# Performance work log

Hardware: AMD Instinct MI355X
Metric: run time of the kernel (lower is better)

Reference implementation:

```python
import jax, jax.numpy as jnp
import numpy as np

B, T, C, NH = 32, 512, 1024, 16
DH = C // NH


def _rope_tables(seq_len, dim):
    # matches RotaryEmbedding: inv_freq over even indices; emb=cat(freqs,freqs),
    # but only the first dim//2 columns (== freqs) are ever sliced out.
    inv = 1.0 / (10000.0 ** (np.arange(0, dim, 2, dtype=np.float32) / dim))
    freqs = np.arange(seq_len, dtype=np.float32)[:, None] * inv[None, :]  # [T, dh/2]
    return jnp.asarray(np.cos(freqs)), jnp.asarray(np.sin(freqs))


def _apply_rope(x, cos, sin):
    # x: [B,T,H,D] with D even; interleaved-pair rotation as in the torch code
    b, t, h, d = x.shape
    d2 = d // 2
    xv = x.reshape(b, t, h, d2, 2)
    x0, x1 = xv[..., 0], xv[..., 1]
    c = cos[None, :t, None, :]  # [1,T,1,d2]
    s = sin[None, :t, None, :]
    o0 = x0 * c - x1 * s
    o1 = x0 * s + x1 * c
    return jnp.stack([o0, o1], axis=-1).reshape(b, t, h, d)


def setup_inputs() -> dict:
    key = jax.random.key(0)
    ks = jax.random.split(key, 5)
    scale = 0.02
    return {
        "x": jax.random.normal(ks[0], (B, T, C), dtype=jnp.float32),
        "Wq": jax.random.normal(ks[1], (C, C), dtype=jnp.float32) * scale,
        "Wk": jax.random.normal(ks[2], (C, C), dtype=jnp.float32) * scale,
        "Wv": jax.random.normal(ks[3], (C, C), dtype=jnp.float32) * scale,
        "Wo": jax.random.normal(ks[4], (C, C), dtype=jnp.float32) * scale,
    }


def reference(x, Wq, Wk, Wv, Wo):
    b, t, c = x.shape
    cos, sin = _rope_tables(t, DH)
    # torch nn.Linear(bias=False): y = x @ W.T
    q = (x @ Wq.T).reshape(b, t, NH, DH)
    k = (x @ Wk.T).reshape(b, t, NH, DH)
    v = (x @ Wv.T).reshape(b, t, NH, DH)
    q = _apply_rope(q, cos, sin)
    k = _apply_rope(k, cos, sin)
    # [B,H,T,D]
    q = q.transpose(0, 2, 1, 3)
    k = k.transpose(0, 2, 1, 3)
    v = v.transpose(0, 2, 1, 3)
    # fp32 scores + fp32 softmax (explicit, matches the torch upcast)
    att = jnp.einsum("bhqd,bhkd->bhqk", q.astype(jnp.float32), k.astype(jnp.float32))
    att = att * (DH ** -0.5)
    att = jax.nn.softmax(att, axis=-1).astype(v.dtype)
    # dropout omitted (eval mode)
    out = jnp.einsum("bhqk,bhkd->bhqd", att, v)
    out = out.transpose(0, 2, 1, 3).reshape(b, t, c)
    return out @ Wo.T
```

## Files before the change

### kernel.cpp

```cpp
#include <hip/hip_runtime.h>
#include <hip/hip_bf16.h>
#include <stdint.h>

#define B_  32
#define T_  512
#define C_  1024
#define NH_ 16
#define DH_ 64

typedef __attribute__((ext_vector_type(8))) __bf16 bf16x8;
typedef __attribute__((ext_vector_type(4))) __bf16 bf16x4;
typedef __attribute__((ext_vector_type(4))) float  f32x4;

__device__ __forceinline__ void gload_lds16(const void* g, void* lds) {
  __builtin_amdgcn_global_load_lds(
      (const __attribute__((address_space(1))) void*)(uintptr_t)g,
      (__attribute__((address_space(3))) void*)(uint32_t)(uintptr_t)lds,
      16, 0, 0);
}

__global__ void prep_kernel(const float* __restrict__ x,
                            const float* __restrict__ Wq, const float* __restrict__ Wk,
                            const float* __restrict__ Wv, const float* __restrict__ Wo,
                            __bf16* __restrict__ xb, __bf16* __restrict__ wqkv,
                            __bf16* __restrict__ wob,
                            float* __restrict__ cosT, float* __restrict__ sinT) {
  int i = blockIdx.x * blockDim.x + threadIdx.x;
  if (i < 4194304) {
    f32x4 v = *(const f32x4*)(x + (size_t)i * 4);
    bf16x4 o;
    o[0] = (__bf16)v[0]; o[1] = (__bf16)v[1]; o[2] = (__bf16)v[2]; o[3] = (__bf16)v[3];
    *(bf16x4*)(xb + (size_t)i * 4) = o;
  } else if (i < 5242880) {
    int j = i - 4194304;
    int w = j >> 18, idx = j & 262143;
    const float* src = (w == 0) ? Wq : (w == 1) ? Wk : (w == 2) ? Wv : Wo;
    __bf16* dst = (w == 3) ? wob : wqkv + (size_t)w * 1048576;
    f32x4 v = *(const f32x4*)(src + (size_t)idx * 4);
    bf16x4 o;
    o[0] = (__bf16)v[0]; o[1] = (__bf16)v[1]; o[2] = (__bf16)v[2]; o[3] = (__bf16)v[3];
    *(bf16x4*)(dst + (size_t)idx * 4) = o;
  } else if (i < 5259264) {
    int j = i - 5242880;
    int t = j >> 5, f = j & 31;
    float inv = powf(10000.0f, -(float)(2 * f) / 64.0f);
    float fr = (float)t * inv;
    cosT[j] = cosf(fr);
    sinT[j] = sinf(fr);
  }
}

template <int MODE>
__global__ __launch_bounds__(512, 2) void gemm8(
    const __bf16* __restrict__ A,
    const __bf16* __restrict__ W0, const __bf16* __restrict__ W1, const __bf16* __restrict__ W2,
    __bf16* __restrict__ q, __bf16* __restrict__ k, __bf16* __restrict__ vt,
    float* __restrict__ outp) {
  extern __shared__ __bf16 lds[];
  const int K = C_;
  const int NH8 = 64;
  int tid = threadIdx.x;
  int lane = tid & 63, wave = tid >> 6;
  int ql = lane & 15, g = lane >> 4;
  int wr = wave >> 2, wc = wave & 3;

  constexpr int BNH = (MODE == 0) ? 6 : 2;
  int bid = blockIdx.x;
  int xcd = bid & 7, local = bid >> 3;
  int bm = (xcd >> 1) * 16 + local / BNH;
  int bn = (xcd & 1) * BNH + local % BNH;

  const __bf16* Ag = A + (size_t)bm * 256 * K;
  const __bf16* Wg;
  if (MODE == 0) {
    int mat = bn >> 2;
    const __bf16* Wsel = (mat == 0) ? W0 : (mat == 1) ? W1 : W2;
    Wg = Wsel + (size_t)(bn & 3) * 256 * K;
  } else {
    Wg = W0 + (size_t)bn * 256 * K;
  }

  int schunk = (tid & 3) ^ ((tid >> 3) & 3);
  size_t stg_base = (size_t)(tid >> 2) * K + schunk * 8;

  int xsw = (g ^ ((ql >> 1) & 3)) * 8;
  int aoffW[8], boffW[4];
#pragma unroll
  for (int m = 0; m < 8; m++) aoffW[m] = (wr * 128 + m * 16 + ql) * 32 + xsw;
#pragma unroll
  for (int n = 0; n < 4; n++) boffW[n] = (wc * 64 + n * 16 + ql) * 32 + xsw;

#define STAGE_H(h)                                                          \
  if ((h) < NH8) {                                                          \
    int tl_ = (h) >> 2, pt_ = (h) & 3;                                      \
    const __bf16* s_ = ((pt_ & 1) ? Wg : Ag) + stg_base +                   \
                       (size_t)tl_ * 64 + (pt_ >> 1) * 32;                  \
    __bf16* d_ = lds + (((tl_ & 1) * 4 + pt_) * 8192) + tid * 8;            \
    gload_lds16(s_, d_);                                                    \
    gload_lds16(s_ + (size_t)128 * K, d_ + 4096);                           \
  }

#define PH(TP, KK, MLO, RB, SH, VM)                                         \
  {                                                                         \
    const __bf16* abase_ = lds + (((TP) * 4 + ((KK) ? 2 : 0)) * 8192);      \
    _Pragma("unroll")                                                       \
    for (int mm = 0; mm < 4; mm++)                                          \
      a[mm] = *(const bf16x8*)(abase_ + aoffW[(MLO) + mm]);                 \
    if (RB) {                                                               \
      const __bf16* bbase_ = lds + (((TP) * 4 + ((KK) ? 3 : 1)) * 8192);    \
      _Pragma("unroll")                                                     \
      for (int n = 0; n < 4; n++)                                           \
        b[n] = *(const bf16x8*)(bbase_ + boffW[n]);                         \
    }                                                                       \
    STAGE_H(SH);                                                            \
    __builtin_amdgcn_s_barrier();                                           \
    asm volatile("s_waitcnt lgkmcnt(0)" ::: "memory");                      \
    __builtin_amdgcn_sched_barrier(0);                                      \
    __builtin_amdgcn_s_setprio(1);                                          \
    _Pragma("unroll")                                                       \
    for (int mm = 0; mm < 4; mm++)                                          \
      _Pragma("unroll")                                                     \
      for (int n = 0; n < 4; n++)                                           \
        acc[(MLO) + mm][n] = __builtin_amdgcn_mfma_f32_16x16x32_bf16(       \
            a[mm], b[n], acc[(MLO) + mm][n], 0, 0, 0);                      \
    __builtin_amdgcn_s_setprio(0);                                          \
    {                                                                       \
      int vm_ = (VM);                                                       \
      if (vm_ == 0)      { asm volatile("s_waitcnt vmcnt(0)" ::: "memory"); } \
      else if (vm_ > 0)  { asm volatile("s_waitcnt vmcnt(6)" ::: "memory"); } \
    }                                                                       \
    __builtin_amdgcn_s_barrier();                                           \
  }

  STAGE_H(0); STAGE_H(1); STAGE_H(2); STAGE_H(3);
  STAGE_H(4); STAGE_H(5); STAGE_H(6);
  asm volatile("s_waitcnt vmcnt(6)" ::: "memory");
  __builtin_amdgcn_s_barrier();
  __builtin_amdgcn_sched_barrier(0);

  f32x4 acc[8][4] = {};
  bf16x8 a[4], b[4];
  for (int i = 0; i < 8; ++i) {
    int hb = 8 * i;
    int vm4 = (i == 7) ? 0 : 6;
    int vm8 = (i == 7) ? -1 : 6;
    PH(0, 0, 0, 1, hb + 7,  -1)
    PH(0, 0, 4, 0, hb + 8,  -1)
    PH(0, 1, 0, 1, hb + 9,  -1)
    PH(0, 1, 4, 0, hb + 10, vm4)
    PH(1, 0, 0, 1, hb + 11, -1)
    PH(1, 0, 4, 0, hb + 12, -1)
    PH(1, 1, 0, 1, hb + 13, -1)
    PH(1, 1, 4, 0, hb + 14, vm8)
  }
#undef PH
#undef STAGE_H

  int r0 = bm * 256 + wr * 128;
  int c0 = bn * 256 + wc * 64;
  if (MODE == 0) {
    int mat = c0 >> 10;
#pragma unroll
    for (int m = 0; m < 8; m++) {
      int row = r0 + m * 16 + g * 4;
      int bb = row >> 9, tt = row & 511;
#pragma unroll
      for (int n = 0; n < 4; n++) {
        int col = c0 + n * 16 + ql;
        int h = (col & 1023) >> 6, d = col & 63;
        if (mat == 2) {
          bf16x4 ov;
#pragma unroll
          for (int r = 0; r < 4; r++) ov[r] = (__bf16)acc[m][n][r];
          *(bf16x4*)(vt + ((size_t)(bb * NH_ + h) * DH_ + d) * T_ + tt) = ov;
        } else {
          __bf16* dst = (mat == 0 ? q : k) + ((size_t)(bb * NH_ + h) * T_ + tt) * DH_ + d;
#pragma unroll
          for (int r = 0; r < 4; r++) dst[r * DH_] = (__bf16)acc[m][n][r];
        }
      }
    }
  } else {
#pragma unroll
    for (int m = 0; m < 8; m++) {
      int row = r0 + m * 16 + g * 4;
#pragma unroll
      for (int r = 0; r < 4; r++)
#pragma unroll
        for (int n = 0; n < 4; n++)
          outp[(size_t)(row + r) * C_ + c0 + n * 16 + ql] = acc[m][n][r];
    }
  }
}

__global__ __launch_bounds__(512, 2) void attn_kernel(
    const __bf16* __restrict__ qg, const __bf16* __restrict__ kg,
    const __bf16* __restrict__ vg, __bf16* __restrict__ ao,
    const float* __restrict__ cosT, const float* __restrict__ sinT) {
  extern __shared__ char smem[];
  __bf16* Klds = (__bf16*)smem;
  __bf16* Vlds = (__bf16*)(smem + 65536);

  int tid = threadIdx.x;
  int lane = tid & 63, wave = tid >> 6;
  int ql = lane & 15, g = lane >> 4;
  int bh = blockIdx.x;
  int b = bh >> 4, h = bh & 15;
  const __bf16* qp = qg + (size_t)bh * (T_ * DH_);
  const __bf16* kp = kg + (size_t)bh * (T_ * DH_);
  const __bf16* vp = vg + (size_t)bh * (T_ * DH_);

  {
    int cb = tid & 7;
    int rb = tid >> 3;
#pragma unroll
    for (int i = 0; i < 8; i++) {
      int row = rb + i * 64;
      bf16x8 raw = *(const bf16x8*)(kp + (size_t)row * DH_ + cb * 8);
      f32x4 c4 = *(const f32x4*)(cosT + row * 32 + cb * 4);
      f32x4 s4 = *(const f32x4*)(sinT + row * 32 + cb * 4);
      bf16x8 out;
#pragma unroll
      for (int p = 0; p < 4; p++) {
        float a0 = (float)raw[2 * p], a1 = (float)raw[2 * p + 1];
        out[2 * p]     = (__bf16)(a0 * c4[p] - a1 * s4[p]);
        out[2 * p + 1] = (__bf16)(a0 * s4[p] + a1 * c4[p]);
      }
      *(bf16x8*)(Klds + row * 64 + ((cb ^ (row & 7)) * 8)) = out;
    }
  }
  {
    int d = tid >> 3;
    int cb = tid & 7;
    const __bf16* vrow = vp + (size_t)d * T_;
#pragma unroll
    for (int i = 0; i < 8; i++) {
      int c8 = cb + i * 8;
      bf16x8 raw = *(const bf16x8*)(vrow + c8 * 8);
      *(bf16x8*)(Vlds + d * 516 + c8 * 8) = raw;
    }
  }

  int q0 = wave * 64;
  bf16x8 qf[4][2];
#pragma unroll
  for (int s = 0; s < 4; s++)
#pragma unroll
    for (int kk = 0; kk < 2; kk++) {
      int tq = q0 + s * 16 + ql;
      bf16x8 raw = *(const bf16x8*)(qp + (size_t)tq * DH_ + kk * 32 + g * 8);
      int fb = tq * 32 + kk * 16 + g * 4;
      f32x4 c4 = *(const f32x4*)(cosT + fb);
      f32x4 s4 = *(const f32x4*)(sinT + fb);
      bf16x8 out;
#pragma unroll
      for (int p = 0; p < 4; p++) {
        float a0 = (float)raw[2 * p], a1 = (float)raw[2 * p + 1];
        out[2 * p]     = (__bf16)(0.125f * (a0 * c4[p] - a1 * s4[p]));
        out[2 * p + 1] = (__bf16)(0.125f * (a0 * s4[p] + a1 * c4[p]));
      }
      qf[s][kk] = out;
    }

  __syncthreads();

  f32x4 o[4][4] = {};
  float mrow[4] = {-1e30f, -1e30f, -1e30f, -1e30f};
  float lrow[4] = {0.f, 0.f, 0.f, 0.f};

  for (int kv0 = 0; kv0 < T_; kv0 += 32) {
    bf16x8 kf[2][2], vf[4];
#pragma unroll
    for (int sub = 0; sub < 2; sub++)
#pragma unroll
      for (int kk = 0; kk < 2; kk++) {
        int t = kv0 + sub * 16 + ql;
        int cc = kk * 4 + g;
        kf[sub][kk] = *(const bf16x8*)(Klds + t * 64 + ((cc ^ (t & 7)) * 8));
      }
#pragma unroll
    for (int c = 0; c < 4; c++) {
      int d = c * 16 + ql;
      bf16x4 vlo = *(const bf16x4*)(Vlds + d * 516 + kv0 + g * 4);
      bf16x4 vhi = *(const bf16x4*)(Vlds + d * 516 + kv0 + 16 + g * 4);
#pragma unroll
      for (int r = 0; r < 4; r++) { vf[c][r] = vlo[r]; vf[c][4 + r] = vhi[r]; }
    }

#pragma unroll
    for (int s = 0; s < 4; s++) {
      f32x4 s0 = {0.f, 0.f, 0.f, 0.f}, s1 = {0.f, 0.f, 0.f, 0.f};
      __builtin_amdgcn_s_setprio(1);
#pragma unroll
      for (int kk = 0; kk < 2; kk++) {
        s0 = __builtin_amdgcn_mfma_f32_16x16x32_bf16(kf[0][kk], qf[s][kk], s0, 0, 0, 0);
        s1 = __builtin_amdgcn_mfma_f32_16x16x32_bf16(kf[1][kk], qf[s][kk], s1, 0, 0, 0);
      }
      __builtin_amdgcn_s_setprio(0);
      float tm = s0[0];
#pragma unroll
      for (int r = 1; r < 4; r++) tm = fmaxf(tm, s0[r]);
#pragma unroll
      for (int r = 0; r < 4; r++) tm = fmaxf(tm, s1[r]);
      tm = fmaxf(tm, __shfl_xor(tm, 16));
      tm = fmaxf(tm, __shfl_xor(tm, 32));
      if (!__all(tm <= mrow[s] + 8.0f)) {
        float mnew = fmaxf(mrow[s], tm);
        float corr = __expf(mrow[s] - mnew);
        mrow[s] = mnew;
        lrow[s] *= corr;
#pragma unroll
        for (int c = 0; c < 4; c++) o[s][c] *= corr;
      }
      float p0[4], p1[4], ps = 0.f;
#pragma unroll
      for (int r = 0; r < 4; r++) {
        p0[r] = __expf(s0[r] - mrow[s]);
        p1[r] = __expf(s1[r] - mrow[s]);
        ps += p0[r] + p1[r];
      }
      ps += __shfl_xor(ps, 16);
      ps += __shfl_xor(ps, 32);
      lrow[s] += ps;
      bf16x8 pb;
#pragma unroll
      for (int r = 0; r < 4; r++) {
        pb[r]     = (__bf16)p0[r];
        pb[4 + r] = (__bf16)p1[r];
      }
      __builtin_amdgcn_s_setprio(1);
#pragma unroll
      for (int c = 0; c < 4; c++)
        o[s][c] = __builtin_amdgcn_mfma_f32_16x16x32_bf16(vf[c], pb, o[s][c], 0, 0, 0);
      __builtin_amdgcn_s_setprio(0);
    }
  }

#pragma unroll
  for (int s = 0; s < 4; s++) {
    float inv = 1.0f / lrow[s];
    size_t row = (size_t)b * T_ + q0 + s * 16 + ql;
    size_t baseo = row * C_ + h * DH_;
#pragma unroll
    for (int c = 0; c < 4; c++) {
      bf16x4 ov;
#pragma unroll
      for (int r = 0; r < 4; r++) ov[r] = (__bf16)(o[s][c][r] * inv);
      *(bf16x4*)(ao + baseo + c * 16 + g * 4) = ov;
    }
  }
}

extern "C" void kernel_launch(void* const* d_in, const int* in_sizes, int n_in,
                              void* d_out, int out_size, void* d_ws, size_t ws_size,
                              hipStream_t stream) {
  (void)in_sizes; (void)n_in; (void)out_size; (void)ws_size;
  const float* x  = (const float*)d_in[0];
  const float* Wq = (const float*)d_in[1];
  const float* Wk = (const float*)d_in[2];
  const float* Wv = (const float*)d_in[3];
  const float* Wo = (const float*)d_in[4];

  char* ws = (char*)d_ws;
  char* od = (char*)d_out;
  float* outp = (float*)d_out;

  __bf16* qb = (__bf16*)(od);
  __bf16* kb = (__bf16*)(od + 33554432);
  __bf16* xb   = (__bf16*)(ws);
  __bf16* vtb  = (__bf16*)(ws + 33554432);
  __bf16* wqkv = (__bf16*)(ws + 67108864);
  __bf16* wob  = (__bf16*)(ws + 73400320);
  float*  cosT = (float*)(ws + 75497472);
  float*  sinT = (float*)(ws + 75563008);
  __bf16* aob  = xb;

  auto k0 = gemm8<0>; auto k1 = gemm8<1>;
  hipFuncSetAttribute((const void*)k0, hipFuncAttributeMaxDynamicSharedMemorySize, 131072);
  hipFuncSetAttribute((const void*)k1, hipFuncAttributeMaxDynamicSharedMemorySize, 131072);
  hipFuncSetAttribute((const void*)attn_kernel, hipFuncAttributeMaxDynamicSharedMemorySize, 131584);

  prep_kernel<<<dim3(20544), dim3(256), 0, stream>>>(
      x, Wq, Wk, Wv, Wo, xb, wqkv, wob, cosT, sinT);

  gemm8<0><<<dim3(768), dim3(512), 131072, stream>>>(
      xb, wqkv, wqkv + 1048576, wqkv + 2097152, qb, kb, vtb, nullptr);

  attn_kernel<<<dim3(B_ * NH_), dim3(512), 131584, stream>>>(
      qb, kb, vtb, aob, cosT, sinT);

  gemm8<1><<<dim3(256), dim3(512), 131072, stream>>>(
      aob, wob, nullptr, nullptr, nullptr, nullptr, nullptr, outp);
}
```

Baseline: 254.8 us.

## Add smaller-tile output projection GEMM and async swizzled V loads in attention

The output projection moves to a new 128x128-tile GEMM kernel with 256 threads, 1024 blocks and XCD-aware block mapping. The aim is better CU occupancy and load balance than the 256-block gemm8<1> launch gave. In attention, V is now staged into LDS with direct global-to-LDS loads using an XOR swizzle instead of a padded row stride, which cuts register round trips and trims LDS to 128 KiB. The new GEMM has no double buffering, so its loads and MFMAs may serialize.

Measured after the change: 265.4 us. 1.04x slower.

```diff
diff --git a/kernel.cpp b/kernel.cpp
--- a/kernel.cpp
+++ b/kernel.cpp
@@ -193,6 +193,68 @@
   }
 }
 
+__global__ __launch_bounds__(256) void gemm_op(
+    const __bf16* __restrict__ A, const __bf16* __restrict__ W,
+    float* __restrict__ outp) {
+  __shared__ __bf16 As[128 * 64];
+  __shared__ __bf16 Bs[128 * 64];
+  const int K = C_;
+  int tid = threadIdx.x;
+  int lane = tid & 63, wave = tid >> 6;
+  int ql = lane & 15, g = lane >> 4;
+  int wr = wave >> 1, wc = wave & 1;
+
+  int xcd = blockIdx.x & 7, local = blockIdx.x >> 3;
+  int bm = xcd * 16 + (local >> 3);
+  int bn = local & 7;
+
+  int srow = tid >> 3;
+  int cphys = tid & 7;
+  int clog = cphys ^ (srow & 7);
+  const __bf16* Ab = A + (size_t)(bm * 128 + srow) * K + clog * 8;
+  const __bf16* Wb = W + (size_t)(bn * 128 + srow) * K + clog * 8;
+  __bf16* AsP = &As[srow * 64 + cphys * 8];
+  __bf16* BsP = &Bs[srow * 64 + cphys * 8];
+
+  int xk = ql & 7;
+  f32x4 acc[4][4] = {};
+  for (int k0 = 0; k0 < K; k0 += 64) {
+#pragma unroll
+    for (int i = 0; i < 4; i++) gload_lds16(Ab + (size_t)i * 32 * K + k0, AsP + i * 2048);
+#pragma unroll
+    for (int i = 0; i < 4; i++) gload_lds16(Wb + (size_t)i * 32 * K + k0, BsP + i * 2048);
+    __syncthreads();
+#pragma unroll
+    for (int kk = 0; kk < 2; kk++) {
+      bf16x8 a[4], b[4];
+#pragma unroll
+      for (int m = 0; m < 4; m++)
+        a[m] = *(const bf16x8*)&As[(wr * 64 + m * 16 + ql) * 64 + (((kk * 4 + g) ^ xk) * 8)];
+#pragma unroll
+      for (int n = 0; n < 4; n++)
+        b[n] = *(const bf16x8*)&Bs[(wc * 64 + n * 16 + ql) * 64 + (((kk * 4 + g) ^ xk) * 8)];
+#pragma unroll
+      for (int m = 0; m < 4; m++)
+#pragma unroll
+        for (int n = 0; n < 4; n++)
+          acc[m][n] = __builtin_amdgcn_mfma_f32_16x16x32_bf16(a[m], b[n], acc[m][n], 0, 0, 0);
+    }
+    __syncthreads();
+  }
+
+  int r0 = bm * 128 + wr * 64;
+  int c0 = bn * 128 + wc * 64;
+#pragma unroll
+  for (int m = 0; m < 4; m++) {
+    int row = r0 + m * 16 + g * 4;
+#pragma unroll
+    for (int r = 0; r < 4; r++)
+#pragma unroll
+      for (int n = 0; n < 4; n++)
+        outp[(size_t)(row + r) * C_ + c0 + n * 16 + ql] = acc[m][n][r];
+  }
+}
+
 __global__ __launch_bounds__(512, 2) void attn_kernel(
     const __bf16* __restrict__ qg, const __bf16* __restrict__ kg,
     const __bf16* __restrict__ vg, __bf16* __restrict__ ao,
@@ -210,6 +272,13 @@
   const __bf16* kp = kg + (size_t)bh * (T_ * DH_);
   const __bf16* vp = vg + (size_t)bh * (T_ * DH_);
 
+#pragma unroll
+  for (int i = 0; i < 8; i++) {
+    int d = i * 8 + wave;
+    const __bf16* src = vp + (size_t)d * T_ + ((lane ^ wave) * 8);
+    gload_lds16(src, Vlds + d * 512 + lane * 8);
+  }
+
   {
     int cb = tid & 7;
     int rb = tid >> 3;
@@ -227,17 +296,6 @@
         out[2 * p + 1] = (__bf16)(a0 * s4[p] + a1 * c4[p]);
       }
       *(bf16x8*)(Klds + row * 64 + ((cb ^ (row & 7)) * 8)) = out;
-    }
-  }
-  {
-    int d = tid >> 3;
-    int cb = tid & 7;
-    const __bf16* vrow = vp + (size_t)d * T_;
-#pragma unroll
-    for (int i = 0; i < 8; i++) {
-      int c8 = cb + i * 8;
-      bf16x8 raw = *(const bf16x8*)(vrow + c8 * 8);
-      *(bf16x8*)(Vlds + d * 516 + c8 * 8) = raw;
     }
   }
 
@@ -281,8 +339,12 @@
 #pragma unroll
     for (int c = 0; c < 4; c++) {
       int d = c * 16 + ql;
-      bf16x4 vlo = *(const bf16x4*)(Vlds + d * 516 + kv0 + g * 4);
-      bf16x4 vhi = *(const bf16x4*)(Vlds + d * 516 + kv0 + 16 + g * 4);
+      int key = ql & 7;
+      const __bf16* vb = Vlds + d * 512;
+      int chlo = ((kv0 >> 3) + (g >> 1)) ^ key;
+      int chhi = (((kv0 + 16) >> 3) + (g >> 1)) ^ key;
+      bf16x4 vlo = *(const bf16x4*)(vb + chlo * 8 + (g & 1) * 4);
+      bf16x4 vhi = *(const bf16x4*)(vb + chhi * 8 + (g & 1) * 4);
 #pragma unroll
       for (int r = 0; r < 4; r++) { vf[c][r] = vlo[r]; vf[c][4 + r] = vhi[r]; }
     }
@@ -375,10 +437,9 @@
   float*  sinT = (float*)(ws + 75563008);
   __bf16* aob  = xb;
 
-  auto k0 = gemm8<0>; auto k1 = gemm8<1>;
+  auto k0 = gemm8<0>;
   hipFuncSetAttribute((const void*)k0, hipFuncAttributeMaxDynamicSharedMemorySize, 131072);
-  hipFuncSetAttribute((const void*)k1, hipFuncAttributeMaxDynamicSharedMemorySize, 131072);
-  hipFuncSetAttribute((const void*)attn_kernel, hipFuncAttributeMaxDynamicSharedMemorySize, 131584);
+  hipFuncSetAttribute((const void*)attn_kernel, hipFuncAttributeMaxDynamicSharedMemorySize, 131072);
 
   prep_kernel<<<dim3(20544), dim3(256), 0, stream>>>(
       x, Wq, Wk, Wv, Wo, xb, wqkv, wob, cosT, sinT);
@@ -386,9 +447,8 @@
   gemm8<0><<<dim3(768), dim3(512), 131072, stream>>>(
       xb, wqkv, wqkv + 1048576, wqkv + 2097152, qb, kb, vtb, nullptr);
 
-  attn_kernel<<<dim3(B_ * NH_), dim3(512), 131584, stream>>>(
+  attn_kernel<<<dim3(B_ * NH_), dim3(512), 131072, stream>>>(
       qb, kb, vtb, aob, cosT, sinT);
 
-  gemm8<1><<<dim3(256), dim3(512), 131072, stream>>>(
-      aob, wob, nullptr, nullptr, nullptr, nullptr, nullptr, outp);
-}
+  gemm_op<<<dim3(1024), dim3(256), 0, stream>>>(aob, wob, outp);
+}
```
